# Performance work log

Measured on AMD Instinct MI355X. Metric: run time of the kernel, lower is better.

Reference implementation:

```python
import jax, jax.numpy as jnp
import numpy as np

N_EMBD = 2048
HEAD_DIM = 128
N_CTX = 2048
BATCH = 8
SEQ = 2048


def setup_inputs() -> dict:
    key = jax.random.key(0)
    ks = jax.random.split(key, 7)
    s = 1.0 / np.sqrt(N_EMBD)
    x = jax.random.normal(ks[0], (BATCH, SEQ, N_EMBD), dtype=jnp.float32)
    # torch Linear params: weight (out, in), bias (out,)
    Wq = jax.random.uniform(ks[1], (HEAD_DIM, N_EMBD), jnp.float32, -s, s)
    bq = jax.random.uniform(ks[2], (HEAD_DIM,), jnp.float32, -s, s)
    Wk = jax.random.uniform(ks[3], (HEAD_DIM, N_EMBD), jnp.float32, -s, s)
    bk = jax.random.uniform(ks[4], (HEAD_DIM,), jnp.float32, -s, s)
    Wv = jax.random.uniform(ks[5], (HEAD_DIM, N_EMBD), jnp.float32, -s, s)
    bv = jax.random.uniform(ks[6], (HEAD_DIM,), jnp.float32, -s, s)
    return {"x": x, "Wq": Wq, "bq": bq, "Wk": Wk, "bk": bk, "Wv": Wv, "bv": bv}


def reference(x, Wq, bq, Wk, bk, Wv, bv):
    # projections: y = x @ W^T + b
    q = jnp.einsum('bse,de->bsd', x, Wq) + bq  # (B, S, D)
    k = jnp.einsum('bse,de->bsd', x, Wk) + bk
    v = jnp.einsum('bse,de->bsd', x, Wv) + bv
    seq = x.shape[1]
    scores = jnp.einsum('bqd,bkd->bqk', q, k)  # (B, S, S)
    # causal mask: strictly-upper-triangular positions set to -inf (before scaling, as in source)
    causal = jnp.triu(jnp.ones((seq, seq), dtype=bool), k=1)
    scores = jnp.where(causal[None, :, :], -jnp.inf, scores)
    # NOTE: source scales by sqrt(seq_size), not sqrt(head_dim)
    weight = jax.nn.softmax(scores / jnp.sqrt(jnp.float32(seq)), axis=-1)
    return jnp.einsum('bqk,bkd->bqd', weight, v)
```

## Files before the change

kernel.cpp:

```cpp
#include <hip/hip_runtime.h>
#include <cmath>

#define BATCH 8
#define SEQ   2048
#define NEMB  2048
#define HD    128
#define NROWS (BATCH * SEQ)

typedef __bf16 v8bf __attribute__((ext_vector_type(8)));
typedef float  f32x4 __attribute__((ext_vector_type(4)));

union U8 { v8bf v; __bf16 b[8]; unsigned short e[8]; };
union F4 { f32x4 v; float f[4]; };

__device__ inline void async16(void* lds, const void* g) {
  __builtin_amdgcn_global_load_lds(
      (const __attribute__((address_space(1))) unsigned int*)g,
      (__attribute__((address_space(3))) unsigned int*)lds, 16, 0, 0);
}

__device__ inline v8bf cvt8(float4 a, float4 b) {
  U8 u;
  u.b[0] = (__bf16)a.x; u.b[1] = (__bf16)a.y; u.b[2] = (__bf16)a.z; u.b[3] = (__bf16)a.w;
  u.b[4] = (__bf16)b.x; u.b[5] = (__bf16)b.y; u.b[6] = (__bf16)b.z; u.b[7] = (__bf16)b.w;
  return u.v;
}

__global__ __launch_bounds__(256) void wpack_kernel(
    const float* __restrict__ Wq, const float* __restrict__ Wk,
    const float* __restrict__ Wv, __bf16* __restrict__ wp) {
  const int g = blockIdx.x * 256 + threadIdx.x;
  const int lane = g & 63;
  const int u = g >> 6;
  const int kk = u & 1;
  const int tt = (u >> 1) & 31;
  const int nf = (u >> 6) & 7;
  const int p  = u >> 9;
  const float* __restrict__ W = p == 0 ? Wq : p == 1 ? Wk : Wv;
  const int row = nf * 16 + (lane & 15);
  const int k   = tt * 64 + kk * 32 + (lane >> 4) * 8;
  const float4* s = (const float4*)(W + (size_t)row * NEMB + k);
  float4 f0 = s[0], f1 = s[1];
  *(v8bf*)(wp + (size_t)g * 8) = cvt8(f0, f1);
}

__global__ __launch_bounds__(512) void qkv_fused_kernel(
    const float* __restrict__ x, const __bf16* __restrict__ Wp,
    const float* __restrict__ bq, const float* __restrict__ bk,
    const float* __restrict__ bv,
    __bf16* __restrict__ Qb, __bf16* __restrict__ Kb, __bf16* __restrict__ Vb)
{
  const int bid0 = blockIdx.x;
  const int mt = ((bid0 & 7) << 5) + (bid0 >> 3);
  const int m0 = mt * 64;

  __shared__ float Asm[2][64 * 64];

  const int t = threadIdx.x, lane = t & 63, w = t >> 6;
  const int wm = w >> 2, wn4 = w & 3;
  const int hi = lane >> 4, lo = lane & 15;

  const float* pa[2];
  int laOff[2];
#pragma unroll
  for (int i = 0; i < 2; ++i) {
    const int j = w * 2 + i;
    const int r = j * 4 + (lane >> 4);
    const int c = (lane & 15) ^ (r & 7);
    pa[i] = x + (size_t)(m0 + r) * NEMB + c * 4;
    laOff[i] = j * 1024;
  }

  const __bf16* bb = Wp + lane * 8;

  f32x4 acc[2][6];
  const f32x4 fz = {0.f, 0.f, 0.f, 0.f};
#pragma unroll
  for (int m = 0; m < 2; ++m)
#pragma unroll
    for (int n = 0; n < 6; ++n) acc[m][n] = fz;

  v8bf B0[6][2], B1[6][2];
  auto LOADB = [&](v8bf (&B)[6][2], int tt) {
#pragma unroll
    for (int n = 0; n < 6; ++n)
#pragma unroll
      for (int kk = 0; kk < 2; ++kk)
        B[n][kk] = *(const v8bf*)(bb + (size_t)((wn4 * 6 + n) * 64 + tt * 2 + kk) * 512);
  };
  auto STAGE_A = [&](int tt, int buf) {
    const int k0 = tt * 64;
    char* base = (char*)&Asm[buf][0];
#pragma unroll
    for (int i = 0; i < 2; ++i) async16(base + laOff[i], pa[i] + k0);
  };
  auto COMPUTE = [&](int buf, v8bf (&B)[6][2]) {
    const char* Ab = (const char*)&Asm[buf][0];
#pragma unroll
    for (int kk = 0; kk < 2; ++kk) {
      v8bf a[2];
#pragma unroll
      for (int m = 0; m < 2; ++m) {
        const int r = wm * 32 + m * 16 + lo;
        const int s = kk * 8 + hi * 2;
        const char* rowp = Ab + r * 256;
        F4 a0, a1;
        a0.v = *(const f32x4*)(rowp + (((s)     ^ (r & 7)) << 4));
        a1.v = *(const f32x4*)(rowp + (((s + 1) ^ (r & 7)) << 4));
        U8 u;
#pragma unroll
        for (int q = 0; q < 4; ++q) {
          u.b[q]     = (__bf16)a0.f[q];
          u.b[q + 4] = (__bf16)a1.f[q];
        }
        a[m] = u.v;
      }
#pragma unroll
      for (int m = 0; m < 2; ++m)
#pragma unroll
        for (int n = 0; n < 6; ++n)
          acc[m][n] = __builtin_amdgcn_mfma_f32_16x16x32_bf16(a[m], B[n][kk], acc[m][n], 0, 0, 0);
    }
  };

  const int NT = NEMB / 64;
  STAGE_A(0, 0);
  LOADB(B0, 0);
  for (int tt = 0; tt < NT; tt += 2) {
    __builtin_amdgcn_s_barrier();
    STAGE_A(tt + 1, 1);
    LOADB(B1, tt + 1);
    asm volatile("s_waitcnt vmcnt(14)" ::: "memory");
    __builtin_amdgcn_s_barrier();
    COMPUTE(0, B0);
    __builtin_amdgcn_s_barrier();
    if (tt + 2 < NT) {
      STAGE_A(tt + 2, 0);
      LOADB(B0, tt + 2);
      asm volatile("s_waitcnt vmcnt(14)" ::: "memory");
    } else {
      asm volatile("s_waitcnt vmcnt(0)" ::: "memory");
    }
    __builtin_amdgcn_s_barrier();
    COMPUTE(1, B1);
  }

#pragma unroll
  for (int n = 0; n < 6; ++n) {
    const int rrb = wn4 * 96 + n * 16;
    const int pj = rrb >> 7;
    const int col = (rrb & 127) + lo;
    __bf16* __restrict__ Out = pj == 0 ? Qb : pj == 1 ? Kb : Vb;
    const float* __restrict__ bias = pj == 0 ? bq : pj == 1 ? bk : bv;
    const float bi = bias[col];
#pragma unroll
    for (int m = 0; m < 2; ++m) {
#pragma unroll
      for (int r = 0; r < 4; ++r) {
        const int row = m0 + wm * 32 + m * 16 + hi * 4 + r;
        Out[(size_t)row * HD + col] = (__bf16)(acc[m][n][r] + bi);
      }
    }
  }
}

__global__ __launch_bounds__(256) void attn_kernel(
    const __bf16* __restrict__ Qb, const __bf16* __restrict__ Kb,
    const __bf16* __restrict__ Vb, __bf16* __restrict__ Opart,
    float* __restrict__ Ml)
{
  const int bid0 = blockIdx.x;
  const int bid = ((bid0 & 7) << 7) + (bid0 >> 3);
  const int b = bid >> 7;
  const int q = bid & 127;
  const int qt = q >> 2;
  const int s  = q & 3;
  const int q0 = qt * 64;
  const int kv_beg = (s * (qt + 1)) >> 2;
  const int kv_end = ((s + 1) * (qt + 1)) >> 2;
  const int nst = kv_end - kv_beg;

  const int t = threadIdx.x, lane = t & 63, w = t >> 6;
  const int hi = lane >> 4, lo = lane & 15;

  __shared__ __bf16 Ksm[2][64 * 128];
  __shared__ __bf16 Vtsm[2][128 * 64];
  __shared__ __bf16 Psm[4][16 * 64];

  v8bf aQ[4];
  {
    const __bf16* qp = Qb + ((size_t)(b * SEQ + q0 + w * 16 + lo)) * HD + hi * 8;
#pragma unroll
    for (int kk = 0; kk < 4; ++kk) aQ[kk] = *(const v8bf*)(qp + kk * 32);
  }

  const __bf16* kga[4];
#pragma unroll
  for (int i = 0; i < 4; ++i) {
    const int r = (w * 4 + i) * 4 + (lane >> 4);
    const int c = (lane & 15) ^ (r & 7);
    kga[i] = Kb + ((size_t)(b * SEQ) + r) * HD + c * 8;
  }

  const int keyg = t >> 4, dg = t & 15;
  U8 vv[4];

  f32x4 accO[8];
  const f32x4 fz = {0.f, 0.f, 0.f, 0.f};
#pragma unroll
  for (int n = 0; n < 8; ++n) accO[n] = fz;
  float m_s[4], l_s[4];
#pragma unroll
  for (int r = 0; r < 4; ++r) { m_s[r] = -INFINITY; l_s[r] = 0.f; }

  const float scale = 0.022097086912079608f;

  if (nst > 0) {
    auto STAGE_K = [&](int kv, int buf) {
      const size_t off = (size_t)kv * 64 * HD;
      char* kb = (char*)&Ksm[buf][0];
#pragma unroll
      for (int i = 0; i < 4; ++i) async16(kb + (w * 4 + i) * 1024, kga[i] + off);
    };
    auto LOAD_V = [&](int kv) {
      const __bf16* vp = Vb + ((size_t)(b * SEQ + kv * 64 + keyg * 4)) * HD + dg * 8;
#pragma unroll
      for (int j = 0; j < 4; ++j) vv[j].v = *(const v8bf*)(vp + (size_t)j * HD);
    };
    auto WRITE_VT = [&](int buf) {
      char* vb2 = (char*)&Vtsm[buf][0];
#pragma unroll
      for (int dd = 0; dd < 8; ++dd) {
        const int d = (dd + dg) & 7;
        ushort4 pk = make_ushort4(vv[0].e[d], vv[1].e[d], vv[2].e[d], vv[3].e[d]);
        const int row = dg * 8 + d;
        *(ushort4*)(vb2 + row * 128 + ((keyg * 8) ^ ((row & 7) << 4))) = pk;
      }
    };

    STAGE_K(kv_beg, 0);
    LOAD_V(kv_beg);
    WRITE_VT(0);
    __syncthreads();

    for (int t2 = 0; t2 < nst; ++t2) {
      const int kv = kv_beg + t2;
      const int cur = t2 & 1;
      const bool more = (t2 + 1 < nst);
      if (more) { STAGE_K(kv + 1, cur ^ 1); LOAD_V(kv + 1); }

      f32x4 accS[4];
#pragma unroll
      for (int n = 0; n < 4; ++n) accS[n] = fz;
      const char* ksm = (const char*)&Ksm[cur][0];
#pragma unroll
      for (int kk = 0; kk < 4; ++kk) {
        const int cb = kk * 64 + hi * 16;
        v8bf bk[4];
#pragma unroll
        for (int n = 0; n < 4; ++n) {
          const int r = n * 16 + lo;
          bk[n] = *(const v8bf*)(ksm + r * 256 + (cb ^ ((r & 7) << 4)));
        }
#pragma unroll
        for (int n = 0; n < 4; ++n)
          accS[n] = __builtin_amdgcn_mfma_f32_16x16x32_bf16(aQ[kk], bk[n], accS[n], 0, 0, 0);
      }

      float sv[4][4];
      const bool diag = (kv == qt);
#pragma unroll
      for (int n = 0; n < 4; ++n)
#pragma unroll
        for (int r = 0; r < 4; ++r) {
          float v = accS[n][r] * scale;
          if (diag) {
            const int key = kv * 64 + n * 16 + lo;
            const int qr = q0 + w * 16 + hi * 4 + r;
            if (key > qr) v = -INFINITY;
          }
          sv[n][r] = v;
        }

      float mx[4];
#pragma unroll
      for (int r = 0; r < 4; ++r) {
        mx[r] = fmaxf(fmaxf(sv[0][r], sv[1][r]), fmaxf(sv[2][r], sv[3][r]));
#pragma unroll
        for (int off = 1; off < 16; off <<= 1)
          mx[r] = fmaxf(mx[r], __shfl_xor(mx[r], off));
      }
      float corr[4], p[4][4], rs[4];
#pragma unroll
      for (int r = 0; r < 4; ++r) {
        const float mnew = fmaxf(m_s[r], mx[r]);
        corr[r] = __expf(m_s[r] - mnew);
        m_s[r] = mnew;
        rs[r] = 0.f;
      }
#pragma unroll
      for (int n = 0; n < 4; ++n)
#pragma unroll
        for (int r = 0; r < 4; ++r) {
          p[n][r] = __expf(sv[n][r] - m_s[r]);
          rs[r] += p[n][r];
        }
#pragma unroll
      for (int r = 0; r < 4; ++r) {
#pragma unroll
        for (int off = 1; off < 16; off <<= 1) rs[r] += __shfl_xor(rs[r], off);
        l_s[r] = l_s[r] * corr[r] + rs[r];
      }
#pragma unroll
      for (int n = 0; n < 8; ++n)
#pragma unroll
        for (int r = 0; r < 4; ++r) accO[n][r] *= corr[r];

#pragma unroll
      for (int n = 0; n < 4; ++n)
#pragma unroll
        for (int r = 0; r < 4; ++r) {
          const int row = hi * 4 + r;
          __bf16 h = (__bf16)p[n][r];
          *(unsigned short*)((char*)&Psm[w][0] + row * 128 +
                             (((n * 16 + lo) * 2) ^ ((row & 7) << 4))) =
              __builtin_bit_cast(unsigned short, h);
        }

      if (more) WRITE_VT(cur ^ 1);

      const char* vsm = (const char*)&Vtsm[cur][0];
#pragma unroll
      for (int k2 = 0; k2 < 2; ++k2) {
        const int cb = k2 * 64 + hi * 16;
        const v8bf aP = *(const v8bf*)((const char*)&Psm[w][0] + lo * 128 + (cb ^ ((lo & 7) << 4)));
#pragma unroll
        for (int n = 0; n < 8; ++n) {
          const int r = n * 16 + lo;
          const v8bf bv = *(const v8bf*)(vsm + r * 128 + (cb ^ ((r & 7) << 4)));
          accO[n] = __builtin_amdgcn_mfma_f32_16x16x32_bf16(aP, bv, accO[n], 0, 0, 0);
        }
      }
      if (more) __syncthreads();
    }
  }

#pragma unroll
  for (int r = 0; r < 4; ++r) {
    const int qr = q0 + w * 16 + hi * 4 + r;
    __bf16* op = Opart + ((size_t)s * NROWS + b * SEQ + qr) * HD + lo;
#pragma unroll
    for (int n = 0; n < 8; ++n) op[n * 16] = (__bf16)accO[n][r];
    if (lo == 0) {
      float* mlp = Ml + ((size_t)s * NROWS + b * SEQ + qr) * 2;
      mlp[0] = m_s[r];
      mlp[1] = l_s[r];
    }
  }
}

__global__ __launch_bounds__(256) void combine_kernel(
    const __bf16* __restrict__ Opart, const float* __restrict__ Ml,
    float* __restrict__ out)
{
  const int idx = blockIdx.x * 256 + threadIdx.x;
  const int row = idx >> 2, ch = idx & 3;
  float m[4], l[4];
#pragma unroll
  for (int s = 0; s < 4; ++s) {
    const float* mlp = Ml + ((size_t)s * NROWS + row) * 2;
    m[s] = mlp[0];
    l[s] = mlp[1];
  }
  const float M = fmaxf(fmaxf(m[0], m[1]), fmaxf(m[2], m[3]));
  float e[4], denom = 0.f;
#pragma unroll
  for (int s = 0; s < 4; ++s) { e[s] = __expf(m[s] - M); denom += l[s] * e[s]; }
  const float inv = 1.f / denom;

  float* po = out + (size_t)row * HD + ch * 32;
#pragma unroll
  for (int j = 0; j < 4; ++j) {
    float sum[8];
#pragma unroll
    for (int q2 = 0; q2 < 8; ++q2) sum[q2] = 0.f;
#pragma unroll
    for (int s = 0; s < 4; ++s) {
      U8 o;
      o.v = *(const v8bf*)(Opart + ((size_t)s * NROWS + row) * HD + ch * 32 + j * 8);
#pragma unroll
      for (int q2 = 0; q2 < 8; ++q2) sum[q2] += (float)o.b[q2] * e[s];
    }
#pragma unroll
    for (int q2 = 0; q2 < 8; ++q2) po[j * 8 + q2] = sum[q2] * inv;
  }
}

extern "C" void kernel_launch(void* const* d_in, const int* in_sizes, int n_in,
                              void* d_out, int out_size, void* d_ws, size_t ws_size,
                              hipStream_t stream) {
  const float* x  = (const float*)d_in[0];
  const float* Wq = (const float*)d_in[1];
  const float* bq = (const float*)d_in[2];
  const float* Wk = (const float*)d_in[3];
  const float* bk = (const float*)d_in[4];
  const float* Wv = (const float*)d_in[5];
  const float* bv = (const float*)d_in[6];
  float* out = (float*)d_out;

  __bf16* Qb = (__bf16*)d_ws;
  __bf16* Kb = Qb + (size_t)NROWS * HD;
  __bf16* Vb = Kb + (size_t)NROWS * HD;
  __bf16* Wp = Vb + (size_t)NROWS * HD;
  __bf16* Opart = Wp + (size_t)1536 * 512;
  float*  Ml = (float*)(Opart + (size_t)4 * NROWS * HD);

  wpack_kernel<<<dim3(384), dim3(256), 0, stream>>>(Wq, Wk, Wv, Wp);
  qkv_fused_kernel<<<dim3(256), dim3(512), 0, stream>>>(
      x, Wp, bq, bk, bv, Qb, Kb, Vb);
  attn_kernel<<<dim3(BATCH * 32 * 4), dim3(256), 0, stream>>>(Qb, Kb, Vb, Opart, Ml);
  combine_kernel<<<dim3(NROWS * 4 / 256), dim3(256), 0, stream>>>(Opart, Ml, out);
}
```

Before: 124.1 us.

## Give each wave a private A staging buffer and drop block barriers in QKV GEMM

```diff
diff --git a/kernel.cpp b/kernel.cpp
--- a/kernel.cpp
+++ b/kernel.cpp
@@ -44,7 +44,7 @@
   *(v8bf*)(wp + (size_t)g * 8) = cvt8(f0, f1);
 }
 
-__global__ __launch_bounds__(512) void qkv_fused_kernel(
+__global__ __launch_bounds__(512, 2) void qkv_fused_kernel(
     const float* __restrict__ x, const __bf16* __restrict__ Wp,
     const float* __restrict__ bq, const float* __restrict__ bk,
     const float* __restrict__ bv,
@@ -54,21 +54,21 @@
   const int mt = ((bid0 & 7) << 5) + (bid0 >> 3);
   const int m0 = mt * 64;
 
-  __shared__ float Asm[2][64 * 64];
+  __shared__ char smem[131072];
 
   const int t = threadIdx.x, lane = t & 63, w = t >> 6;
   const int wm = w >> 2, wn4 = w & 3;
   const int hi = lane >> 4, lo = lane & 15;
 
-  const float* pa[2];
-  int laOff[2];
-#pragma unroll
-  for (int i = 0; i < 2; ++i) {
-    const int j = w * 2 + i;
-    const int r = j * 4 + (lane >> 4);
-    const int c = (lane & 15) ^ (r & 7);
-    pa[i] = x + (size_t)(m0 + r) * NEMB + c * 4;
-    laOff[i] = j * 1024;
+  char* const Abuf0 = smem + w * 16384;
+  char* const Abuf1 = Abuf0 + 8192;
+
+  const float* pa[8];
+#pragma unroll
+  for (int i = 0; i < 8; ++i) {
+    const int rl = i * 4 + (lane >> 4);
+    const int c = (lane & 15) ^ (rl & 7);
+    pa[i] = x + (size_t)(m0 + wm * 32 + rl) * NEMB + c * 4;
   }
 
   const __bf16* bb = Wp + lane * 8;
@@ -88,25 +88,23 @@
       for (int kk = 0; kk < 2; ++kk)
         B[n][kk] = *(const v8bf*)(bb + (size_t)((wn4 * 6 + n) * 64 + tt * 2 + kk) * 512);
   };
-  auto STAGE_A = [&](int tt, int buf) {
+  auto STAGE_A = [&](int tt, char* Ab) {
     const int k0 = tt * 64;
-    char* base = (char*)&Asm[buf][0];
-#pragma unroll
-    for (int i = 0; i < 2; ++i) async16(base + laOff[i], pa[i] + k0);
+#pragma unroll
+    for (int i = 0; i < 8; ++i) async16(Ab + i * 1024, pa[i] + k0);
   };
-  auto COMPUTE = [&](int buf, v8bf (&B)[6][2]) {
-    const char* Ab = (const char*)&Asm[buf][0];
+  auto COMPUTE = [&](const char* Ab, v8bf (&B)[6][2]) {
 #pragma unroll
     for (int kk = 0; kk < 2; ++kk) {
       v8bf a[2];
 #pragma unroll
       for (int m = 0; m < 2; ++m) {
-        const int r = wm * 32 + m * 16 + lo;
+        const int rl = m * 16 + lo;
         const int s = kk * 8 + hi * 2;
-        const char* rowp = Ab + r * 256;
+        const char* rowp = Ab + rl * 256;
         F4 a0, a1;
-        a0.v = *(const f32x4*)(rowp + (((s)     ^ (r & 7)) << 4));
-        a1.v = *(const f32x4*)(rowp + (((s + 1) ^ (r & 7)) << 4));
+        a0.v = *(const f32x4*)(rowp + (((s)     ^ (rl & 7)) << 4));
+        a1.v = *(const f32x4*)(rowp + (((s + 1) ^ (rl & 7)) << 4));
         U8 u;
 #pragma unroll
         for (int q = 0; q < 4; ++q) {
@@ -124,25 +122,23 @@
   };
 
   const int NT = NEMB / 64;
-  STAGE_A(0, 0);
+  STAGE_A(0, Abuf0);
   LOADB(B0, 0);
   for (int tt = 0; tt < NT; tt += 2) {
-    __builtin_amdgcn_s_barrier();
-    STAGE_A(tt + 1, 1);
+    STAGE_A(tt + 1, Abuf1);
     LOADB(B1, tt + 1);
-    asm volatile("s_waitcnt vmcnt(14)" ::: "memory");
-    __builtin_amdgcn_s_barrier();
-    COMPUTE(0, B0);
-    __builtin_amdgcn_s_barrier();
+    asm volatile("s_waitcnt vmcnt(20)" ::: "memory");
+    __builtin_amdgcn_sched_barrier(0);
+    COMPUTE(Abuf0, B0);
     if (tt + 2 < NT) {
-      STAGE_A(tt + 2, 0);
+      STAGE_A(tt + 2, Abuf0);
       LOADB(B0, tt + 2);
-      asm volatile("s_waitcnt vmcnt(14)" ::: "memory");
+      asm volatile("s_waitcnt vmcnt(20)" ::: "memory");
     } else {
       asm volatile("s_waitcnt vmcnt(0)" ::: "memory");
     }
-    __builtin_amdgcn_s_barrier();
-    COMPUTE(1, B1);
+    __builtin_amdgcn_sched_barrier(0);
+    COMPUTE(Abuf1, B1);
   }
 
 #pragma unroll
```

Result: no change. 123.4 us (-0.6%).
